# Kernel tuning notes

Measured on AMD Instinct MI355X. Metric: run time of the kernel, lower is better.

The kernel has to match this reference:

```python
import jax, jax.numpy as jnp
import numpy as np

N, D, H, E = 50000, 64, 4, 400000
LN_EPS = 1e-5


def setup_inputs() -> dict:
    key = jax.random.key(0)
    ks = jax.random.split(key, 8)
    x = jax.random.normal(ks[0], (N, D), dtype=jnp.float32)
    edge_index = jax.random.randint(ks[1], (2, E), 0, N, dtype=jnp.int64)
    # nn.Linear(dim, dim*heads, bias=False): weight shape (H*D, D)
    W_lin = jax.random.normal(ks[2], (H * D, D), dtype=jnp.float32) * (1.0 / np.sqrt(D))
    attn_src = jax.random.normal(ks[3], (H, D), dtype=jnp.float32) * 0.1
    attn_dst = jax.random.normal(ks[4], (H, D), dtype=jnp.float32) * 0.1
    # nn.Linear(dim*heads, dim): weight (D, H*D), bias (D,)
    W_out = jax.random.normal(ks[5], (D, H * D), dtype=jnp.float32) * (1.0 / np.sqrt(H * D))
    b_out = jnp.zeros((D,), dtype=jnp.float32)
    ln_g = jnp.ones((D,), dtype=jnp.float32)
    ln_b = jnp.zeros((D,), dtype=jnp.float32)
    return {"x": x, "edge_index": edge_index, "W_lin": W_lin,
            "attn_src": attn_src, "attn_dst": attn_dst,
            "W_out": W_out, "b_out": b_out, "ln_g": ln_g, "ln_b": ln_b}


def reference(x, edge_index, W_lin, attn_src, attn_dst, W_out, b_out, ln_g, ln_b):
    n = x.shape[0]
    i, j = edge_index[0], edge_index[1]  # dst, src node ids per edge
    xh = (x @ W_lin.T).reshape(n, H, D)                 # [N,H,D]
    # per-node attention contributions (equivalent to per-edge dot in source)
    s_dst = jnp.einsum('nhd,hd->nh', xh, attn_dst)      # [N,H]
    s_src = jnp.einsum('nhd,hd->nh', xh, attn_src)      # [N,H]
    alpha = jax.nn.leaky_relu(s_dst[i] + s_src[j], 0.2) # [E,H]
    alpha_exp = jnp.exp(alpha)                          # source uses raw exp (no max-shift)
    denom = jax.ops.segment_sum(alpha_exp, i, num_segments=n)  # [N,H]
    attn = alpha_exp / (denom[i] + 1e-9)                # [E,H]
    msg = attn[:, :, None] * xh[j]                      # [E,H,D]
    out = jax.ops.segment_sum(msg, i, num_segments=n)   # [N,H,D]
    out = out.reshape(n, H * D) @ W_out.T + b_out       # [N,D]
    y = jax.nn.elu(out) + x
    mu = jnp.mean(y, axis=-1, keepdims=True)
    var = jnp.mean(jnp.square(y - mu), axis=-1, keepdims=True)
    return (y - mu) * jax.lax.rsqrt(var + LN_EPS) * ln_g + ln_b
```

## Files before the change

### kernel.cpp

```cpp
#include <hip/hip_runtime.h>

#define N_NODES 50000
#define DIM     64
#define HEADS   4
#define NEDGES  400000
#define HD      256
#define MAXDEG  32
#define NPREP   200
#define ZSTRIDE 264

typedef _Float16 half2v __attribute__((ext_vector_type(2)));
typedef _Float16 half4v __attribute__((ext_vector_type(4)));
typedef _Float16 half8v __attribute__((ext_vector_type(8)));
typedef float    f32x4  __attribute__((ext_vector_type(4)));

union EU { int2 i2; half4v h; };

__global__ __launch_bounds__(256) void k_prep(
    const float* __restrict__ x,
    const float* __restrict__ W_lin,
    const float* __restrict__ attn_src,
    const float* __restrict__ attn_dst,
    const float* __restrict__ W_out,
    _Float16* __restrict__ G2T,
    _Float16* __restrict__ x16,
    float* __restrict__ S,
    int* __restrict__ cnt)
{
    __shared__ float weffsh[512];
    const int b = blockIdx.x, t = threadIdx.x;

    for (int id = t; id < 512; id += 256) {
        const int sd = id >> 8, rem = id & 255, h = rem >> 6, k = rem & 63;
        const float* av = sd ? attn_dst : attn_src;
        float acc = 0.f;
        for (int d = 0; d < DIM; ++d)
            acc = fmaf(av[h * DIM + d], W_lin[(h * DIM + d) * DIM + k], acc);
        weffsh[id] = acc;
    }

    for (int idx = b * 256 + t; idx < N_NODES; idx += NPREP * 256)
        cnt[idx] = 0;

    {
        const int id = b * 256 + t;
        if (id < 64 * 256) {
            const int d = id >> 8, rem = id & 255, m = rem >> 2, h = rem & 3;
            float acc = 0.f;
            for (int k = 0; k < DIM; ++k)
                acc = fmaf(W_lin[(h * DIM + k) * DIM + m],
                           W_out[d * HD + h * DIM + k], acc);
            G2T[d * HD + m * 4 + h] = (_Float16)acc;
        }
    }
    __syncthreads();

    for (int base = b * 32; base < N_NODES; base += NPREP * 32) {
        const int ni = base + (t >> 3);
        if (ni < N_NODES) {
            const int combo = t & 7;
            const float4* xr = (const float4*)(x + (size_t)ni * DIM);
            const float4* wr = (const float4*)(weffsh + combo * DIM);
            float acc = 0.f;
#pragma unroll
            for (int kp = 0; kp < 16; ++kp) {
                const float4 a = xr[kp], bw = wr[kp];
                acc = fmaf(a.x, bw.x, acc);
                acc = fmaf(a.y, bw.y, acc);
                acc = fmaf(a.z, bw.z, acc);
                acc = fmaf(a.w, bw.w, acc);
            }
            S[(size_t)ni * 8 + combo] = acc;
        }
        const size_t e0 = (size_t)base * DIM + (size_t)t * 8;
        if (e0 + 8 <= (size_t)N_NODES * DIM) {
            const float4 u = *(const float4*)(x + e0);
            const float4 v = *(const float4*)(x + e0 + 4);
            half8v hv;
            hv[0]=(_Float16)u.x; hv[1]=(_Float16)u.y; hv[2]=(_Float16)u.z; hv[3]=(_Float16)u.w;
            hv[4]=(_Float16)v.x; hv[5]=(_Float16)v.y; hv[6]=(_Float16)v.z; hv[7]=(_Float16)v.w;
            *(half8v*)(x16 + e0) = hv;
        }
    }
}

__global__ __launch_bounds__(256) void k_edge(
    const int* __restrict__ ei,
    const float* __restrict__ S,
    int* __restrict__ cnt,
    int4* __restrict__ bucketE)
{
    const int e = blockIdx.x * 256 + threadIdx.x;
    if (e >= NEDGES) return;
    const int i = ei[e];
    const int j = ei[NEDGES + e];
    const float4 sd = *(const float4*)(S + (size_t)i * 8 + 4);
    const float4 ss = *(const float4*)(S + (size_t)j * 8);
    float u;
    u = sd.x + ss.x; u = u > 0.f ? u : 0.2f * u; const float e0 = __expf(u);
    u = sd.y + ss.y; u = u > 0.f ? u : 0.2f * u; const float e1 = __expf(u);
    u = sd.z + ss.z; u = u > 0.f ? u : 0.2f * u; const float e2 = __expf(u);
    u = sd.w + ss.w; u = u > 0.f ? u : 0.2f * u; const float e3 = __expf(u);
    EU pk;
    pk.h[0] = (_Float16)e0; pk.h[1] = (_Float16)e1;
    pk.h[2] = (_Float16)e2; pk.h[3] = (_Float16)e3;
    int4 ent;
    ent.x = j; ent.y = pk.i2.x; ent.z = pk.i2.y; ent.w = 0;
    const int slot = atomicAdd(&cnt[i], 1);
    if (slot < MAXDEG) bucketE[(size_t)i * MAXDEG + slot] = ent;
}

__global__ __launch_bounds__(256) void k_ga(
    const int* __restrict__ cnt,
    const int4* __restrict__ bucketE,
    const _Float16* __restrict__ x16,
    const _Float16* __restrict__ G2T,
    const float* __restrict__ b_out,
    const float* __restrict__ ln_g,
    const float* __restrict__ ln_b,
    float* __restrict__ out)
{
    __shared__ _Float16 znsh[16 * ZSTRIDE];
    __shared__ float ysh[16][65];

    const int t = threadIdx.x, wv = t >> 6, l = t & 63;
    const int n0 = blockIdx.x * 16;
    const int side = l >> 5, p = l & 31;

    const int4 degv = *(const int4*)(cnt + n0 + wv * 4);
    int degs[4] = {degv.x, degv.y, degv.z, degv.w};
    int4 E[4];
#pragma unroll
    for (int r = 0; r < 4; ++r)
        E[r] = bucketE[(size_t)(n0 + wv * 4 + r) * MAXDEG + p];

#pragma unroll
    for (int r = 0; r < 4; ++r) {
        const int deg = degs[r] < MAXDEG ? degs[r] : MAXDEG;

        float za0=0.f, za1=0.f, za2=0.f, za3=0.f;
        float zb0=0.f, zb1=0.f, zb2=0.f, zb3=0.f;
        float d0=0.f, d1=0.f, d2=0.f, d3=0.f;

        for (int s = 0; s < deg; s += 8) {
            int jj[4], ey[4], ez[4];
#pragma unroll
            for (int q = 0; q < 4; ++q) {
                const int ss = s + 2 * q + side;
                const int jv = __shfl(E[r].x, ss, 64);
                const int yv = __shfl(E[r].y, ss, 64);
                const int zv = __shfl(E[r].z, ss, 64);
                const bool v = ss < deg;
                jj[q] = v ? jv : 0;
                ey[q] = v ? yv : 0;
                ez[q] = v ? zv : 0;
            }
            half2v xv[4];
#pragma unroll
            for (int q = 0; q < 4; ++q)
                xv[q] = *(const half2v*)(x16 + (size_t)jj[q] * DIM + p * 2);
#pragma unroll
            for (int q = 0; q < 4; ++q) {
                EU u; u.i2 = make_int2(ey[q], ez[q]);
                const float e0 = (float)u.h[0], e1 = (float)u.h[1];
                const float e2 = (float)u.h[2], e3 = (float)u.h[3];
                d0 += e0; d1 += e1; d2 += e2; d3 += e3;
                const float fa = (float)xv[q][0], fb = (float)xv[q][1];
                za0 = fmaf(e0, fa, za0); za1 = fmaf(e1, fa, za1);
                za2 = fmaf(e2, fa, za2); za3 = fmaf(e3, fa, za3);
                zb0 = fmaf(e0, fb, zb0); zb1 = fmaf(e1, fb, zb1);
                zb2 = fmaf(e2, fb, zb2); zb3 = fmaf(e3, fb, zb3);
            }
        }

        d0 += __shfl_xor(d0, 32, 64); d1 += __shfl_xor(d1, 32, 64);
        d2 += __shfl_xor(d2, 32, 64); d3 += __shfl_xor(d3, 32, 64);
        za0 += __shfl_xor(za0, 32, 64); za1 += __shfl_xor(za1, 32, 64);
        za2 += __shfl_xor(za2, 32, 64); za3 += __shfl_xor(za3, 32, 64);
        zb0 += __shfl_xor(zb0, 32, 64); zb1 += __shfl_xor(zb1, 32, 64);
        zb2 += __shfl_xor(zb2, 32, 64); zb3 += __shfl_xor(zb3, 32, 64);

        const float r0 = 1.f / (d0 + 1e-9f), r1 = 1.f / (d1 + 1e-9f);
        const float r2 = 1.f / (d2 + 1e-9f), r3 = 1.f / (d3 + 1e-9f);
        if (side == 0) {
            half8v o;
            o[0] = (_Float16)(za0 * r0); o[1] = (_Float16)(za1 * r1);
            o[2] = (_Float16)(za2 * r2); o[3] = (_Float16)(za3 * r3);
            o[4] = (_Float16)(zb0 * r0); o[5] = (_Float16)(zb1 * r1);
            o[6] = (_Float16)(zb2 * r2); o[7] = (_Float16)(zb3 * r3);
            *(half8v*)(znsh + (wv * 4 + r) * ZSTRIDE + p * 8) = o;
        }
    }
    __syncthreads();

    const int mrow = l & 15, quad = l >> 4;
    half8v A[8];
    const _Float16* zr = znsh + mrow * ZSTRIDE + quad * 8;
#pragma unroll
    for (int s = 0; s < 8; ++s)
        A[s] = *(const half8v*)(zr + 32 * s);

    const _Float16* gp = G2T + (size_t)(wv * 16 + mrow) * HD + quad * 8;
    f32x4 c = {0.f, 0.f, 0.f, 0.f};
#pragma unroll
    for (int s = 0; s < 8; ++s)
        c = __builtin_amdgcn_mfma_f32_16x16x32_f16(A[s], *(const half8v*)(gp + 32 * s), c, 0, 0, 0);

    const int col = wv * 16 + mrow;
    const float bo = b_out[col];
#pragma unroll
    for (int rho = 0; rho < 4; ++rho) {
        const int nl = quad * 4 + rho;
        const float o = c[rho] + bo;
        const float eo = o > 0.f ? o : expm1f(o);
        ysh[nl][col] = eo + (float)x16[(size_t)(n0 + nl) * DIM + col];
    }
    __syncthreads();

    const float g = ln_g[l], bb = ln_b[l];
#pragma unroll
    for (int r = 0; r < 4; ++r) {
        const int nl = wv * 4 + r;
        const float y = ysh[nl][l];
        float sum = y;
#pragma unroll
        for (int off = 32; off > 0; off >>= 1) sum += __shfl_xor(sum, off, 64);
        const float mu = sum * (1.f / 64.f);
        const float dy = y - mu;
        float vs = dy * dy;
#pragma unroll
        for (int off = 32; off > 0; off >>= 1) vs += __shfl_xor(vs, off, 64);
        const float rr = rsqrtf(vs * (1.f / 64.f) + 1e-5f);
        out[(size_t)(n0 + nl) * DIM + l] = dy * rr * g + bb;
    }
}

extern "C" void kernel_launch(void* const* d_in, const int* in_sizes, int n_in,
                              void* d_out, int out_size, void* d_ws, size_t ws_size,
                              hipStream_t stream)
{
    const float* x        = (const float*)d_in[0];
    const int*   ei       = (const int*)d_in[1];
    const float* W_lin    = (const float*)d_in[2];
    const float* attn_src = (const float*)d_in[3];
    const float* attn_dst = (const float*)d_in[4];
    const float* W_out    = (const float*)d_in[5];
    const float* b_out    = (const float*)d_in[6];
    const float* ln_g     = (const float*)d_in[7];
    const float* ln_b     = (const float*)d_in[8];
    float* out = (float*)d_out;

    char* ws = (char*)d_ws;
    _Float16* x16    = (_Float16*)ws;
    float*    S      = (float*)(x16 + (size_t)N_NODES * DIM);
    _Float16* G2T    = (_Float16*)(S + (size_t)N_NODES * 8);
    int*      cnt    = (int*)(G2T + 64 * HD);
    int4*     bucketE= (int4*)(cnt + N_NODES);

    k_prep<<<NPREP, 256, 0, stream>>>(x, W_lin, attn_src, attn_dst, W_out,
                                      G2T, x16, S, cnt);

    k_edge<<<(NEDGES + 255) / 256, 256, 0, stream>>>(ei, S, cnt, bucketE);

    k_ga<<<N_NODES / 16, 256, 0, stream>>>(cnt, bucketE, x16, G2T,
                                           b_out, ln_g, ln_b, out);
}
```

Before: 162.9 us.

## Software-pipeline neighbor gathers across rows and process two edges per thread

```diff
diff --git a/kernel.cpp b/kernel.cpp
--- a/kernel.cpp
+++ b/kernel.cpp
@@ -4,6 +4,7 @@
 #define DIM     64
 #define HEADS   4
 #define NEDGES  400000
+#define EHALF   200000
 #define HD      256
 #define MAXDEG  32
 #define NPREP   200
@@ -91,23 +92,38 @@
     int4* __restrict__ bucketE)
 {
     const int e = blockIdx.x * 256 + threadIdx.x;
-    if (e >= NEDGES) return;
-    const int i = ei[e];
-    const int j = ei[NEDGES + e];
-    const float4 sd = *(const float4*)(S + (size_t)i * 8 + 4);
-    const float4 ss = *(const float4*)(S + (size_t)j * 8);
+    if (e >= EHALF) return;
+    const int i0 = ei[e],         j0 = ei[NEDGES + e];
+    const int i1 = ei[EHALF + e], j1 = ei[NEDGES + EHALF + e];
+    const float4 sd0 = *(const float4*)(S + (size_t)i0 * 8 + 4);
+    const float4 ss0 = *(const float4*)(S + (size_t)j0 * 8);
+    const float4 sd1 = *(const float4*)(S + (size_t)i1 * 8 + 4);
+    const float4 ss1 = *(const float4*)(S + (size_t)j1 * 8);
     float u;
-    u = sd.x + ss.x; u = u > 0.f ? u : 0.2f * u; const float e0 = __expf(u);
-    u = sd.y + ss.y; u = u > 0.f ? u : 0.2f * u; const float e1 = __expf(u);
-    u = sd.z + ss.z; u = u > 0.f ? u : 0.2f * u; const float e2 = __expf(u);
-    u = sd.w + ss.w; u = u > 0.f ? u : 0.2f * u; const float e3 = __expf(u);
-    EU pk;
-    pk.h[0] = (_Float16)e0; pk.h[1] = (_Float16)e1;
-    pk.h[2] = (_Float16)e2; pk.h[3] = (_Float16)e3;
-    int4 ent;
-    ent.x = j; ent.y = pk.i2.x; ent.z = pk.i2.y; ent.w = 0;
-    const int slot = atomicAdd(&cnt[i], 1);
-    if (slot < MAXDEG) bucketE[(size_t)i * MAXDEG + slot] = ent;
+    u = sd0.x + ss0.x; u = u > 0.f ? u : 0.2f * u; const float a0 = __expf(u);
+    u = sd0.y + ss0.y; u = u > 0.f ? u : 0.2f * u; const float a1 = __expf(u);
+    u = sd0.z + ss0.z; u = u > 0.f ? u : 0.2f * u; const float a2 = __expf(u);
+    u = sd0.w + ss0.w; u = u > 0.f ? u : 0.2f * u; const float a3 = __expf(u);
+    u = sd1.x + ss1.x; u = u > 0.f ? u : 0.2f * u; const float b0 = __expf(u);
+    u = sd1.y + ss1.y; u = u > 0.f ? u : 0.2f * u; const float b1 = __expf(u);
+    u = sd1.z + ss1.z; u = u > 0.f ? u : 0.2f * u; const float b2 = __expf(u);
+    u = sd1.w + ss1.w; u = u > 0.f ? u : 0.2f * u; const float b3 = __expf(u);
+
+    EU pk0; pk0.h[0]=(_Float16)a0; pk0.h[1]=(_Float16)a1;
+            pk0.h[2]=(_Float16)a2; pk0.h[3]=(_Float16)a3;
+    EU pk1; pk1.h[0]=(_Float16)b0; pk1.h[1]=(_Float16)b1;
+            pk1.h[2]=(_Float16)b2; pk1.h[3]=(_Float16)b3;
+
+    const int s0 = atomicAdd(&cnt[i0], 1);
+    const int s1 = atomicAdd(&cnt[i1], 1);
+    if (s0 < MAXDEG) {
+        int4 ent; ent.x = j0; ent.y = pk0.i2.x; ent.z = pk0.i2.y; ent.w = 0;
+        bucketE[(size_t)i0 * MAXDEG + s0] = ent;
+    }
+    if (s1 < MAXDEG) {
+        int4 ent; ent.x = j1; ent.y = pk1.i2.x; ent.z = pk1.i2.y; ent.w = 0;
+        bucketE[(size_t)i1 * MAXDEG + s1] = ent;
+    }
 }
 
 __global__ __launch_bounds__(256) void k_ga(
@@ -128,68 +144,87 @@
     const int side = l >> 5, p = l & 31;
 
     const int4 degv = *(const int4*)(cnt + n0 + wv * 4);
-    int degs[4] = {degv.x, degv.y, degv.z, degv.w};
+    int degc[4];
+    degc[0] = degv.x < MAXDEG ? degv.x : MAXDEG;
+    degc[1] = degv.y < MAXDEG ? degv.y : MAXDEG;
+    degc[2] = degv.z < MAXDEG ? degv.z : MAXDEG;
+    degc[3] = degv.w < MAXDEG ? degv.w : MAXDEG;
     int4 E[4];
 #pragma unroll
     for (int r = 0; r < 4; ++r)
         E[r] = bucketE[(size_t)(n0 + wv * 4 + r) * MAXDEG + p];
 
+    auto issue_group = [&](int r, int s, int deg, int* jjo, half2v* xvo) {
+#pragma unroll
+        for (int q = 0; q < 4; ++q) {
+            const int ss = s + 2 * q + side;
+            const int jv = __shfl(E[r].x, ss, 64);
+            jjo[q] = (ss < deg) ? jv : 0;
+        }
+#pragma unroll
+        for (int q = 0; q < 4; ++q)
+            xvo[q] = *(const half2v*)(x16 + (size_t)jjo[q] * DIM + p * 2);
+    };
+
+    int jjc[4]; half2v xvc[4];
+    issue_group(0, 0, degc[0], jjc, xvc);
+
 #pragma unroll
     for (int r = 0; r < 4; ++r) {
-        const int deg = degs[r] < MAXDEG ? degs[r] : MAXDEG;
-
-        float za0=0.f, za1=0.f, za2=0.f, za3=0.f;
-        float zb0=0.f, zb1=0.f, zb2=0.f, zb3=0.f;
-        float d0=0.f, d1=0.f, d2=0.f, d3=0.f;
-
-        for (int s = 0; s < deg; s += 8) {
-            int jj[4], ey[4], ez[4];
+        int jjn[4]; half2v xvn[4];
+        if (r < 3) issue_group(r + 1, 0, degc[r + 1], jjn, xvn);
+
+        float za[4] = {0.f, 0.f, 0.f, 0.f};
+        float zb[4] = {0.f, 0.f, 0.f, 0.f};
+        float dd[4] = {0.f, 0.f, 0.f, 0.f};
+
+        auto consume_group = [&](int s, const half2v* xv) {
 #pragma unroll
             for (int q = 0; q < 4; ++q) {
                 const int ss = s + 2 * q + side;
-                const int jv = __shfl(E[r].x, ss, 64);
-                const int yv = __shfl(E[r].y, ss, 64);
-                const int zv = __shfl(E[r].z, ss, 64);
-                const bool v = ss < deg;
-                jj[q] = v ? jv : 0;
-                ey[q] = v ? yv : 0;
-                ez[q] = v ? zv : 0;
-            }
-            half2v xv[4];
-#pragma unroll
-            for (int q = 0; q < 4; ++q)
-                xv[q] = *(const half2v*)(x16 + (size_t)jj[q] * DIM + p * 2);
-#pragma unroll
-            for (int q = 0; q < 4; ++q) {
-                EU u; u.i2 = make_int2(ey[q], ez[q]);
+                int ey = __shfl(E[r].y, ss, 64);
+                int ez = __shfl(E[r].z, ss, 64);
+                const bool v = ss < degc[r];
+                ey = v ? ey : 0;
+                ez = v ? ez : 0;
+                EU u; u.i2 = make_int2(ey, ez);
                 const float e0 = (float)u.h[0], e1 = (float)u.h[1];
                 const float e2 = (float)u.h[2], e3 = (float)u.h[3];
-                d0 += e0; d1 += e1; d2 += e2; d3 += e3;
+                dd[0] += e0; dd[1] += e1; dd[2] += e2; dd[3] += e3;
                 const float fa = (float)xv[q][0], fb = (float)xv[q][1];
-                za0 = fmaf(e0, fa, za0); za1 = fmaf(e1, fa, za1);
-                za2 = fmaf(e2, fa, za2); za3 = fmaf(e3, fa, za3);
-                zb0 = fmaf(e0, fb, zb0); zb1 = fmaf(e1, fb, zb1);
-                zb2 = fmaf(e2, fb, zb2); zb3 = fmaf(e3, fb, zb3);
+                za[0] = fmaf(e0, fa, za[0]); za[1] = fmaf(e1, fa, za[1]);
+                za[2] = fmaf(e2, fa, za[2]); za[3] = fmaf(e3, fa, za[3]);
+                zb[0] = fmaf(e0, fb, zb[0]); zb[1] = fmaf(e1, fb, zb[1]);
+                zb[2] = fmaf(e2, fb, zb[2]); zb[3] = fmaf(e3, fb, zb[3]);
             }
-        }
-
-        d0 += __shfl_xor(d0, 32, 64); d1 += __shfl_xor(d1, 32, 64);
-        d2 += __shfl_xor(d2, 32, 64); d3 += __shfl_xor(d3, 32, 64);
-        za0 += __shfl_xor(za0, 32, 64); za1 += __shfl_xor(za1, 32, 64);
-        za2 += __shfl_xor(za2, 32, 64); za3 += __shfl_xor(za3, 32, 64);
-        zb0 += __shfl_xor(zb0, 32, 64); zb1 += __shfl_xor(zb1, 32, 64);
-        zb2 += __shfl_xor(zb2, 32, 64); zb3 += __shfl_xor(zb3, 32, 64);
-
-        const float r0 = 1.f / (d0 + 1e-9f), r1 = 1.f / (d1 + 1e-9f);
-        const float r2 = 1.f / (d2 + 1e-9f), r3 = 1.f / (d3 + 1e-9f);
+        };
+
+        consume_group(0, xvc);
+        for (int s = 8; s < degc[r]; s += 8) {
+            int jr[4]; half2v xr[4];
+            issue_group(r, s, degc[r], jr, xr);
+            consume_group(s, xr);
+        }
+
+#pragma unroll
+        for (int h = 0; h < 4; ++h) {
+            dd[h] += __shfl_xor(dd[h], 32, 64);
+            za[h] += __shfl_xor(za[h], 32, 64);
+            zb[h] += __shfl_xor(zb[h], 32, 64);
+        }
+        const float r0 = 1.f / (dd[0] + 1e-9f), r1 = 1.f / (dd[1] + 1e-9f);
+        const float r2 = 1.f / (dd[2] + 1e-9f), r3 = 1.f / (dd[3] + 1e-9f);
         if (side == 0) {
             half8v o;
-            o[0] = (_Float16)(za0 * r0); o[1] = (_Float16)(za1 * r1);
-            o[2] = (_Float16)(za2 * r2); o[3] = (_Float16)(za3 * r3);
-            o[4] = (_Float16)(zb0 * r0); o[5] = (_Float16)(zb1 * r1);
-            o[6] = (_Float16)(zb2 * r2); o[7] = (_Float16)(zb3 * r3);
+            o[0] = (_Float16)(za[0] * r0); o[1] = (_Float16)(za[1] * r1);
+            o[2] = (_Float16)(za[2] * r2); o[3] = (_Float16)(za[3] * r3);
+            o[4] = (_Float16)(zb[0] * r0); o[5] = (_Float16)(zb[1] * r1);
+            o[6] = (_Float16)(zb[2] * r2); o[7] = (_Float16)(zb[3] * r3);
             *(half8v*)(znsh + (wv * 4 + r) * ZSTRIDE + p * 8) = o;
         }
+
+#pragma unroll
+        for (int q = 0; q < 4; ++q) { jjc[q] = jjn[q]; xvc[q] = xvn[q]; }
     }
     __syncthreads();
 
@@ -260,7 +295,7 @@
     k_prep<<<NPREP, 256, 0, stream>>>(x, W_lin, attn_src, attn_dst, W_out,
                                       G2T, x16, S, cnt);
 
-    k_edge<<<(NEDGES + 255) / 256, 256, 0, stream>>>(ei, S, cnt, bucketE);
+    k_edge<<<(EHALF + 255) / 256, 256, 0, stream>>>(ei, S, cnt, bucketE);
 
     k_ga<<<N_NODES / 16, 256, 0, stream>>>(cnt, bucketE, x16, G2T,
                                            b_out, ln_g, ln_b, out);
```

After: 160.8 us. About the same (-1.3%).
